# Kernel tuning notes

Hardware: AMD Instinct MI355X
Metric: run time of the kernel (lower is better)

## Reference

```python
import jax, jax.numpy as jnp
import numpy as np

HEADS = 16
DIM_HEAD = 64
SCALE = DIM_HEAD ** -0.5


def setup_inputs() -> dict:
    key = jax.random.key(0)
    ks = jax.random.split(key, 5)
    B, N, D = 2, 2048, 1024  # query_dim = inner_dim = 1024
    s = 0.02
    return {
        "x": jax.random.normal(ks[0], (B, N, D), dtype=jnp.float32),
        "Wq": jax.random.normal(ks[1], (D, D), dtype=jnp.float32) * s,
        "Wk": jax.random.normal(ks[2], (D, D), dtype=jnp.float32) * s,
        "Wv": jax.random.normal(ks[3], (D, D), dtype=jnp.float32) * s,
        "Wout": jax.random.normal(ks[4], (D, D), dtype=jnp.float32) * s,
        "bout": jnp.zeros((D,), dtype=jnp.float32),
    }


def reference(x, Wq, Wk, Wv, Wout, bout):
    B, N, D = x.shape
    h, dh = HEADS, DIM_HEAD
    # projections (torch Linear: y = x @ W.T); context = x (self-attention)
    q = (x @ Wq.T).reshape(B, N, h, dh).transpose(0, 2, 1, 3)  # b h n d
    k = (x @ Wk.T).reshape(B, N, h, dh).transpose(0, 2, 1, 3)
    v = (x @ Wv.T).reshape(B, N, h, dh).transpose(0, 2, 1, 3)
    # scaled dot-product attention; chunk loop in original is math-equivalent
    s = jnp.einsum('bhid,bhjd->bhij', q, k) * SCALE
    p = jax.nn.softmax(s, axis=-1)
    o = jnp.einsum('bhij,bhjd->bhid', p, v)  # b h n d
    o = o.transpose(0, 2, 1, 3).reshape(B, N, h * dh)
    return o @ Wout.T + bout
```

## Files before the change

kernel.cpp:

```cpp
#include <hip/hip_runtime.h>
#include <stdint.h>

using bf16x8 = __attribute__((ext_vector_type(8))) short;
using f32x4  = __attribute__((ext_vector_type(4))) float;
using s16x4  = __attribute__((ext_vector_type(4))) short;

__device__ __forceinline__ short f2bf(float f) {
    union { float f; uint32_t u; } v; v.f = f;
    uint32_t u = v.u;
    uint32_t r = (u + 0x7fffu + ((u >> 16) & 1u)) >> 16;
    return (short)r;
}

__device__ __forceinline__ uint32_t cvtpk_bf16(float a, float b) {
    uint32_t r;
    asm("v_cvt_pk_bf16_f32 %0, %1, %2" : "=v"(r) : "v"(a), "v"(b));
    return r;
}

__device__ __forceinline__ void gload_lds16(const void* g, void* l) {
    __builtin_amdgcn_global_load_lds(
        reinterpret_cast<const uint32_t __attribute__((address_space(1)))*>(
            reinterpret_cast<uintptr_t>(g)),
        reinterpret_cast<uint32_t __attribute__((address_space(3)))*>(
            reinterpret_cast<uintptr_t>(l)),
        16, 0, 0);
}

__global__ __launch_bounds__(256) void cvt_all(
    const float* __restrict__ x, const float* __restrict__ wq,
    const float* __restrict__ wk, const float* __restrict__ wv,
    const float* __restrict__ wo,
    short* __restrict__ xb, short* __restrict__ wqb, short* __restrict__ wkb,
    short* __restrict__ wvb, short* __restrict__ wob)
{
    int i = blockIdx.x * 256 + threadIdx.x;
    const float* src; short* dst; int off;
    if      (i < 1048576) { src = x;  dst = xb;  off = i; }
    else if (i < 1310720) { src = wq; dst = wqb; off = i - 1048576; }
    else if (i < 1572864) { src = wk; dst = wkb; off = i - 1310720; }
    else if (i < 1835008) { src = wv; dst = wvb; off = i - 1572864; }
    else                  { src = wo; dst = wob; off = i - 1835008; }
    float4 f = ((const float4*)src)[off];
    s16x4 r; r[0] = f2bf(f.x); r[1] = f2bf(f.y); r[2] = f2bf(f.z); r[3] = f2bf(f.w);
    ((s16x4*)dst)[off] = r;
}

template <bool IS_OUT>
__global__ __launch_bounds__(256) void gemm_bt(
    const short* __restrict__ A,
    const short* __restrict__ Bq, const short* __restrict__ Bk,
    const short* __restrict__ Bv,
    short* __restrict__ qb, short* __restrict__ kb, short* __restrict__ vtb,
    float* __restrict__ outp, const float* __restrict__ bias)
{
    constexpr int BN = IS_OUT ? 64 : 128;
    constexpr int BC = BN / 32;
    constexpr int NI = BN / 32;
    __shared__ short As[2][128 * 64];
    __shared__ short Bs[2][BN * 64];
    const int tid  = threadIdx.x;
    const int wave = tid >> 6, lane = tid & 63;
    const int lo = lane & 15, hi = lane >> 4;

    const int nwg = gridDim.x * gridDim.y * gridDim.z;
    int lin = blockIdx.x + blockIdx.y * gridDim.x +
              blockIdx.z * gridDim.x * gridDim.y;
    const int s = (lin & 7) * (nwg >> 3) + (lin >> 3);
    const int m_base = IS_OUT ? ((s >> 4) & 31) * 128 : ((s >> 3) & 31) * 128;
    const int n_base = IS_OUT ? (s & 15) * 64        : (s & 7) * 128;
    const int z = IS_OUT ? 0 : (s >> 8);

    const short* Bw = IS_OUT ? Bq : (z == 0 ? Bq : (z == 1 ? Bk : Bv));
    const int wr = wave >> 1, wc = wave & 1;

    f32x4 acc[4][NI];
#pragma unroll
    for (int i = 0; i < 4; ++i)
#pragma unroll
        for (int j = 0; j < NI; ++j) acc[i][j] = (f32x4){0.f, 0.f, 0.f, 0.f};

    const int se = (lane & 7) * 8;
    const short* Ag = A  + (size_t)(m_base + wave * 32 + (lane >> 3)) * 1024 + se;
    const short* Bg = Bw + (size_t)(n_base + wave * (BN / 4) + (lane >> 3)) * 1024 + se;

    auto GSTAGE = [&](int kt) {
        const int k0 = kt * 64, bf = kt & 1;
#pragma unroll
        for (int c = 0; c < 4; ++c)
            gload_lds16(Ag + (size_t)c * 8 * 1024 + k0, &As[bf][(wave * 32 + c * 8) * 64]);
#pragma unroll
        for (int c = 0; c < BC; ++c)
            gload_lds16(Bg + (size_t)c * 8 * 1024 + k0,
                        &Bs[bf][(wave * (BN / 4) + c * 8) * 64]);
    };

    GSTAGE(0);
    for (int kt = 0; kt < 16; ++kt) {
        if (kt < 15) {
            GSTAGE(kt + 1);
            if constexpr (IS_OUT)
                asm volatile("s_waitcnt vmcnt(6)" ::: "memory");
            else
                asm volatile("s_waitcnt vmcnt(8)" ::: "memory");
        } else {
            asm volatile("s_waitcnt vmcnt(0)" ::: "memory");
        }
        __builtin_amdgcn_s_barrier();
        const int bf = kt & 1;
#pragma unroll
        for (int ks = 0; ks < 2; ++ks) {
            bf16x8 av[4], bv[NI];
#pragma unroll
            for (int i = 0; i < 4; ++i)
                av[i] = *(const bf16x8*)&As[bf][(wr * 64 + i * 16 + lo) * 64 + ks * 32 + hi * 8];
#pragma unroll
            for (int i = 0; i < NI; ++i)
                bv[i] = *(const bf16x8*)&Bs[bf][(wc * (BN / 2) + i * 16 + lo) * 64 + ks * 32 + hi * 8];
#pragma unroll
            for (int mi = 0; mi < 4; ++mi)
#pragma unroll
                for (int ni = 0; ni < NI; ++ni)
                    acc[mi][ni] = __builtin_amdgcn_mfma_f32_16x16x32_bf16(
                        av[mi], bv[ni], acc[mi][ni], 0, 0, 0);
        }
        asm volatile("s_waitcnt lgkmcnt(0)" ::: "memory");
        __builtin_amdgcn_s_barrier();
    }

#pragma unroll
    for (int mi = 0; mi < 4; ++mi) {
#pragma unroll
        for (int ni = 0; ni < NI; ++ni) {
            const int n = n_base + wc * (BN / 2) + ni * 16 + lo;
            if (IS_OUT) {
                const float bsv = bias[n];
#pragma unroll
                for (int i = 0; i < 4; ++i) {
                    const int m = m_base + wr * 64 + mi * 16 + hi * 4 + i;
                    outp[(size_t)m * 1024 + n] = acc[mi][ni][i] + bsv;
                }
            } else {
                const int h = n >> 6, d = n & 63;
                if (z == 2) {
                    const int m0 = m_base + wr * 64 + mi * 16 + hi * 4;
                    const int b = m0 >> 11, ns = m0 & 2047;
                    const int k6 = ns & 63;
                    const int nsp = (ns & ~63) | (k6 & 0x20) |
                                    ((k6 & 0x10) >> 2) | ((k6 & 0x0C) << 1);
                    s16x4 pk;
#pragma unroll
                    for (int i = 0; i < 4; ++i) pk[i] = f2bf(acc[mi][ni][i]);
                    *(s16x4*)&vtb[(((size_t)b * 16 + h) * 64 + d) * 2048 + nsp] = pk;
                } else {
                    short* dstp = (z == 0) ? qb : kb;
                    const float scl = (z == 0) ? 0.18033688011112042f : 1.0f;
#pragma unroll
                    for (int i = 0; i < 4; ++i) {
                        const int m = m_base + wr * 64 + mi * 16 + hi * 4 + i;
                        const int b = m >> 11, ns = m & 2047;
                        dstp[(((size_t)b * 16 + h) * 2048 + ns) * 64 + d] =
                            f2bf(acc[mi][ni][i] * scl);
                    }
                }
            }
        }
    }
}


#define QKT16B_(BUFN, S) do {                                                  \
    const char* kb_ = (const char*)K_lds[BUFN];                                \
    bf16x8 kf_[4];                                                             \
    _Pragma("unroll")                                                          \
    for (int mi = 0; mi < 4; ++mi)                                             \
        kf_[mi] = *(const bf16x8*)(kb_ + koff0 + mi * 2048);                   \
    _Pragma("unroll")                                                          \
    for (int mi = 0; mi < 4; ++mi)                                             \
        _Pragma("unroll")                                                      \
        for (int nf = 0; nf < 2; ++nf)                                         \
            S[mi][nf] = __builtin_amdgcn_mfma_f32_16x16x32_bf16(               \
                kf_[mi], qf[nf][0], Z4, 0, 0, 0);                              \
    _Pragma("unroll")                                                          \
    for (int mi = 0; mi < 4; ++mi)                                             \
        kf_[mi] = *(const bf16x8*)(kb_ + koff1 + mi * 2048);                   \
    _Pragma("unroll")                                                          \
    for (int mi = 0; mi < 4; ++mi)                                             \
        _Pragma("unroll")                                                      \
        for (int nf = 0; nf < 2; ++nf)                                         \
            S[mi][nf] = __builtin_amdgcn_mfma_f32_16x16x32_bf16(               \
                kf_[mi], qf[nf][1], S[mi][nf], 0, 0, 0);                       \
    } while (0)

#define STAGE_(T_, BUF_) do {                                                  \
    const size_t go_ = (size_t)(T_) * gstep;                                   \
    _Pragma("unroll")                                                          \
    for (int c = 0; c < 4; ++c) {                                              \
        void* dst_ = (stV == 0) ? (void*)&K_lds[BUF_][(rbase + c * 8) * 64]    \
                                : (void*)&V_lds[BUF_][(rbase + c * 8) * 64];   \
        gload_lds16(gp[c] + go_, dst_);                                        \
    } } while (0)

#define HALF16_(T, SC, SN, DOQ, BUFC, BUFN, BUFS, DOS) do {                    \
    asm volatile("s_waitcnt vmcnt(0)" ::: "memory");                           \
    __builtin_amdgcn_s_barrier();                                              \
    if (DOQ) {                                                                 \
        __builtin_amdgcn_s_setprio(1);                                         \
        QKT16B_(BUFN, SN);                                                     \
        __builtin_amdgcn_s_setprio(0);                                         \
    }                                                                          \
    if (DOS) STAGE_((T) + 2, BUFS);            \
                          \
    float pm_[2];                                                              \
    _Pragma("unroll")                                                          \
    for (int nf = 0; nf < 2; ++nf) {                                           \
        float a0 = fmaxf(fmaxf(SC[0][nf][0], SC[0][nf][1]),                    \
                         fmaxf(SC[0][nf][2], SC[0][nf][3]));                   \
        float a1 = fmaxf(fmaxf(SC[1][nf][0], SC[1][nf][1]),                    \
                         fmaxf(SC[1][nf][2], SC[1][nf][3]));                   \
        float a2 = fmaxf(fmaxf(SC[2][nf][0], SC[2][nf][1]),                    \
                         fmaxf(SC[2][nf][2], SC[2][nf][3]));                   \
        float a3 = fmaxf(fmaxf(SC[3][nf][0], SC[3][nf][1]),                    \
                         fmaxf(SC[3][nf][2], SC[3][nf][3]));                   \
        pm_[nf] = fmaxf(fmaxf(a0, a1), fmaxf(a2, a3));                         \
    }                                                                          \
    const int keep_ = (pm_[0] <= mrow[0] + 8.f) && (pm_[1] <= mrow[1] + 8.f);  \
    if (!__all(keep_)) {                  \
        float alpha_[2];                                                       \
        _Pragma("unroll")                                                      \
        for (int nf = 0; nf < 2; ++nf) {                                       \
            float m4 = pm_[nf];                                                \
            m4 = fmaxf(m4, __shfl_xor(m4, 16));                                \
            m4 = fmaxf(m4, __shfl_xor(m4, 32));                                \
            const float mn = fmaxf(mrow[nf], m4);                              \
            alpha_[nf] = __builtin_amdgcn_exp2f(mrow[nf] - mn);                \
            mrow[nf]  = mn;                                                    \
            lrow[nf] *= alpha_[nf];                                            \
        }                                                                      \
        _Pragma("unroll")                                                      \
        for (int mi = 0; mi < 2; ++mi)                                         \
            _Pragma("unroll")                                                  \
            for (int i = 0; i < 4; ++i) {                                      \
                const float av = __shfl(alpha_[mi], hi * 4 + i);               \
                _Pragma("unroll")                                              \
                for (int nf = 0; nf < 4; ++nf) oacc[mi][nf][i] *= av;          \
            }                                                                  \
    }                                                                          \
    _Pragma("unroll")                                                          \
    for (int nf = 0; nf < 2; ++nf) {        \
        float s0 = 0.f, s1 = 0.f, s2 = 0.f, s3 = 0.f;                          \
        _Pragma("unroll")                                                      \
        for (int mi = 0; mi < 4; ++mi) {                                       \
            SC[mi][nf][0] = __builtin_amdgcn_exp2f(SC[mi][nf][0] - mrow[nf]);  \
            s0 += SC[mi][nf][0];                                               \
            SC[mi][nf][1] = __builtin_amdgcn_exp2f(SC[mi][nf][1] - mrow[nf]);  \
            s1 += SC[mi][nf][1];                                               \
            SC[mi][nf][2] = __builtin_amdgcn_exp2f(SC[mi][nf][2] - mrow[nf]);  \
            s2 += SC[mi][nf][2];                                               \
            SC[mi][nf][3] = __builtin_amdgcn_exp2f(SC[mi][nf][3] - mrow[nf]);  \
            s3 += SC[mi][nf][3];                                               \
        }                                                                      \
        lrow[nf] += (s0 + s1) + (s2 + s3);                                     \
    }                                                                          \
                 \
    uint32_t W2_[4][2][2];                                                     \
    _Pragma("unroll")                                                          \
    for (int mi = 0; mi < 4; ++mi)                                             \
        _Pragma("unroll")                                                      \
        for (int nf = 0; nf < 2; ++nf) {                                       \
            W2_[mi][nf][0] = cvtpk_bf16(SC[mi][nf][0], SC[mi][nf][1]);         \
            W2_[mi][nf][1] = cvtpk_bf16(SC[mi][nf][2], SC[mi][nf][3]);         \
        }                                                                      \
           \
    __builtin_amdgcn_s_setprio(1);                                             \
    _Pragma("unroll")                                                          \
    for (int ks = 0; ks < 2; ++ks) {                                           \
        const char* vb_ = (const char*)V_lds[BUFC];                            \
        bf16x8 vf_[4];                                                         \
        _Pragma("unroll")                                                      \
        for (int nf = 0; nf < 4; ++nf)                                         \
            vf_[nf] = *(const bf16x8*)(vb_ + (ks ? koff1 : koff0) + nf * 2048);\
        _Pragma("unroll")                                                      \
        for (int mo = 0; mo < 2; ++mo) {                                       \
            union { uint32_t u[4]; bf16x8 v; } pk_;                            \
            pk_.u[0] = W2_[ks * 2][mo][0];     pk_.u[1] = W2_[ks * 2][mo][1];  \
            pk_.u[2] = W2_[ks * 2 + 1][mo][0]; pk_.u[3] = W2_[ks * 2 + 1][mo][1]; \
            _Pragma("unroll")                                                  \
            for (int nf = 0; nf < 4; ++nf)                                     \
                oacc[mo][nf] = __builtin_amdgcn_mfma_f32_16x16x32_bf16(        \
                    pk_.v, vf_[nf], oacc[mo][nf], 0, 0, 0);                    \
        }                                                                      \
    }                                                                          \
    __builtin_amdgcn_s_setprio(0);                                             \
    } while (0)

__global__ __launch_bounds__(256) void attn(
    const short* __restrict__ qg, const short* __restrict__ kg,
    const short* __restrict__ vtg, short* __restrict__ ob)
{
    __shared__ short K_lds[3][64 * 64];
    __shared__ short V_lds[3][64 * 64];

    const int tid  = threadIdx.x;
    const int wave = tid >> 6, lane = tid & 63;
    const int lo = lane & 15, hi = lane >> 4;
    const int koff0 = lo * 128 + ((hi ^ (lo & 7)) << 4);
    const int koff1 = koff0 ^ 64;

    int bid = blockIdx.y * 16 + blockIdx.x;
    bid = (bid & 7) * 64 + (bid >> 3);
    const int bh = bid >> 4;
    const int qw = (bid & 15) * 128 + wave * 32;

    bf16x8 qf[2][2];
#pragma unroll
    for (int nf = 0; nf < 2; ++nf)
#pragma unroll
        for (int ks = 0; ks < 2; ++ks)
            qf[nf][ks] = *(const bf16x8*)&qg[((size_t)bh * 2048 + qw + nf * 16 + lo) * 64 +
                                             ks * 32 + hi * 8];
    asm volatile("s_waitcnt vmcnt(0)" ::: "memory");

    f32x4 oacc[2][4];
#pragma unroll
    for (int mi = 0; mi < 2; ++mi)
#pragma unroll
        for (int nf = 0; nf < 4; ++nf) oacc[mi][nf] = (f32x4){0.f, 0.f, 0.f, 0.f};
    float mrow[2] = {-1e30f, -1e30f};
    float lrow[2] = {0.f, 0.f};
    const f32x4 Z4 = (f32x4){0.f, 0.f, 0.f, 0.f};

    const short* kgb = kg  + (size_t)bh * 2048 * 64;
    const short* vgb = vtg + (size_t)bh * 64 * 2048;

    const int stV = wave >> 1, rbase = (wave & 1) * 32;
    const short* gp[4];
#pragma unroll
    for (int c = 0; c < 4; ++c) {
        const int r  = rbase + c * 8 + (lane >> 3);
        const int sg = (lane & 7) ^ (r & 7);
        gp[c] = (stV == 0) ? (kgb + (size_t)r * 64 + sg * 8)
                           : (vgb + (size_t)r * 2048 + sg * 8);
    }
    const int gstep = (stV == 0) ? 4096 : 64;

    STAGE_(0, 0); STAGE_(1, 1);

    f32x4 sA[4][2], sB[4][2];

    asm volatile("s_waitcnt vmcnt(4)" ::: "memory");
    __builtin_amdgcn_s_barrier();
    QKT16B_(0, sA);

    for (int tb = 0; tb < 30; tb += 6) {
        HALF16_(tb + 0, sA, sB, 1, 0, 1, 2, 1);
        HALF16_(tb + 1, sB, sA, 1, 1, 2, 0, 1);
        HALF16_(tb + 2, sA, sB, 1, 2, 0, 1, 1);
        HALF16_(tb + 3, sB, sA, 1, 0, 1, 2, 1);
        HALF16_(tb + 4, sA, sB, 1, 1, 2, 0, 1);
        HALF16_(tb + 5, sB, sA, 1, 2, 0, 1, 1);
    }
    HALF16_(30, sA, sB, 1, 0, 1, 2, 0);
    HALF16_(31, sB, sA, 0, 1, 2, 0, 0);

    float lfull[2];
#pragma unroll
    for (int nf = 0; nf < 2; ++nf) {
        float ts = lrow[nf];
        ts += __shfl_xor(ts, 16);
        ts += __shfl_xor(ts, 32);
        lfull[nf] = ts;
    }
    const int b = bh >> 4, h = bh & 15;
#pragma unroll
    for (int mi = 0; mi < 2; ++mi)
#pragma unroll
        for (int i = 0; i < 4; ++i) {
            const float lv = __shfl(lfull[mi], hi * 4 + i);
            const float r  = 1.0f / lv;
            const int qrow = qw + mi * 16 + hi * 4 + i;
#pragma unroll
            for (int nf = 0; nf < 4; ++nf)
                ob[((size_t)b * 2048 + qrow) * 1024 + h * 64 + nf * 16 + lo] =
                    f2bf(oacc[mi][nf][i] * r);
        }
}

extern "C" void kernel_launch(void* const* d_in, const int* in_sizes, int n_in,
                              void* d_out, int out_size, void* d_ws, size_t ws_size,
                              hipStream_t stream) {
    const float* x   = (const float*)d_in[0];
    const float* Wq  = (const float*)d_in[1];
    const float* Wk  = (const float*)d_in[2];
    const float* Wv  = (const float*)d_in[3];
    const float* Wo  = (const float*)d_in[4];
    const float* bo  = (const float*)d_in[5];
    float* outp = (float*)d_out;

    char* ws = (char*)d_ws;
    short* xb  = (short*)(ws);
    short* qb  = (short*)(ws + (8u  << 20));
    short* kb  = (short*)(ws + (16u << 20));
    short* vtb = (short*)(ws + (24u << 20));
    short* ob  = (short*)(ws + (32u << 20));
    short* wqb = (short*)(ws + (40u << 20));
    short* wkb = (short*)(ws + (42u << 20));
    short* wvb = (short*)(ws + (44u << 20));
    short* wob = (short*)(ws + (46u << 20));

    cvt_all<<<8192, 256, 0, stream>>>(x, Wq, Wk, Wv, Wo, xb, wqb, wkb, wvb, wob);
    gemm_bt<false><<<dim3(8, 32, 3), 256, 0, stream>>>(
        xb, wqb, wkb, wvb, qb, kb, vtb, nullptr, nullptr);
    attn<<<dim3(16, 32), 256, 0, stream>>>(qb, kb, vtb, ob);
    gemm_bt<true><<<dim3(16, 32, 1), 256, 0, stream>>>(
        ob, wob, nullptr, nullptr, nullptr, nullptr, nullptr, outp, bo);
}
```

Measured before the change: 123.6 us.

## Decouple K and V staging with a shorter V prefetch distance

K and V tiles now load through separate staging macros. K keeps a triple buffer prefetched two iterations ahead, while V uses a double buffer prefetched one iteration ahead. This cuts LDS use (one fewer V buffer) and may allow higher occupancy, but V loads have less time to land before they are consumed. The buffer index schedule in the unrolled loop is rewritten to match.

```diff
diff --git a/kernel.cpp b/kernel.cpp
--- a/kernel.cpp
+++ b/kernel.cpp
@@ -192,24 +192,32 @@
                 kf_[mi], qf[nf][1], S[mi][nf], 0, 0, 0);                       \
     } while (0)
 
-#define STAGE_(T_, BUF_) do {                                                  \
-    const size_t go_ = (size_t)(T_) * gstep;                                   \
-    _Pragma("unroll")                                                          \
-    for (int c = 0; c < 4; ++c) {                                              \
-        void* dst_ = (stV == 0) ? (void*)&K_lds[BUF_][(rbase + c * 8) * 64]    \
-                                : (void*)&V_lds[BUF_][(rbase + c * 8) * 64];   \
-        gload_lds16(gp[c] + go_, dst_);                                        \
+#define STAGEK_(T_, BUF_) do {                                                 \
+    if (stV == 0) {                                                            \
+        const size_t go_ = (size_t)(T_) * 4096;                                \
+        _Pragma("unroll")                                                      \
+        for (int c = 0; c < 4; ++c)                                            \
+            gload_lds16(gp[c] + go_, &K_lds[BUF_][(rbase + c * 8) * 64]);      \
     } } while (0)
 
-#define HALF16_(T, SC, SN, DOQ, BUFC, BUFN, BUFS, DOS) do {                    \
+#define STAGEV_(T_, BUF_) do {                                                 \
+    if (stV == 1) {                                                            \
+        const size_t go_ = (size_t)(T_) * 64;                                  \
+        _Pragma("unroll")                                                      \
+        for (int c = 0; c < 4; ++c)                                            \
+            gload_lds16(gp[c] + go_, &V_lds[BUF_][(rbase + c * 8) * 64]);      \
+    } } while (0)
+
+#define HALF16_(T, SC, SN, DOQ, BUFCV, BUFNK, BUFSK, BUFSV, DOSK, DOSV) do {   \
     asm volatile("s_waitcnt vmcnt(0)" ::: "memory");                           \
     __builtin_amdgcn_s_barrier();                                              \
     if (DOQ) {                                                                 \
         __builtin_amdgcn_s_setprio(1);                                         \
-        QKT16B_(BUFN, SN);                                                     \
+        QKT16B_(BUFNK, SN);                                                    \
         __builtin_amdgcn_s_setprio(0);                                         \
     }                                                                          \
-    if (DOS) STAGE_((T) + 2, BUFS);            \
+    if (DOSK) STAGEK_((T) + 2, BUFSK);         \
+    if (DOSV) STAGEV_((T) + 1, BUFSV);                                         \
                           \
     float pm_[2];                                                              \
     _Pragma("unroll")                                                          \
@@ -275,7 +283,7 @@
     __builtin_amdgcn_s_setprio(1);                                             \
     _Pragma("unroll")                                                          \
     for (int ks = 0; ks < 2; ++ks) {                                           \
-        const char* vb_ = (const char*)V_lds[BUFC];                            \
+        const char* vb_ = (const char*)V_lds[BUFCV];                           \
         bf16x8 vf_[4];                                                         \
         _Pragma("unroll")                                                      \
         for (int nf = 0; nf < 4; ++nf)                                         \
@@ -299,7 +307,7 @@
     const short* __restrict__ vtg, short* __restrict__ ob)
 {
     __shared__ short K_lds[3][64 * 64];
-    __shared__ short V_lds[3][64 * 64];
+    __shared__ short V_lds[2][64 * 64];
 
     const int tid  = threadIdx.x;
     const int wave = tid >> 6, lane = tid & 63;
@@ -342,9 +350,8 @@
         gp[c] = (stV == 0) ? (kgb + (size_t)r * 64 + sg * 8)
                            : (vgb + (size_t)r * 2048 + sg * 8);
     }
-    const int gstep = (stV == 0) ? 4096 : 64;
-
-    STAGE_(0, 0); STAGE_(1, 1);
+
+    STAGEK_(0, 0); STAGEV_(0, 0); STAGEK_(1, 1);
 
     f32x4 sA[4][2], sB[4][2];
 
@@ -353,15 +360,15 @@
     QKT16B_(0, sA);
 
     for (int tb = 0; tb < 30; tb += 6) {
-        HALF16_(tb + 0, sA, sB, 1, 0, 1, 2, 1);
-        HALF16_(tb + 1, sB, sA, 1, 1, 2, 0, 1);
-        HALF16_(tb + 2, sA, sB, 1, 2, 0, 1, 1);
-        HALF16_(tb + 3, sB, sA, 1, 0, 1, 2, 1);
-        HALF16_(tb + 4, sA, sB, 1, 1, 2, 0, 1);
-        HALF16_(tb + 5, sB, sA, 1, 2, 0, 1, 1);
+        HALF16_(tb + 0, sA, sB, 1, 0, 1, 2, 1, 1, 1);
+        HALF16_(tb + 1, sB, sA, 1, 1, 2, 0, 0, 1, 1);
+        HALF16_(tb + 2, sA, sB, 1, 0, 0, 1, 1, 1, 1);
+        HALF16_(tb + 3, sB, sA, 1, 1, 1, 2, 0, 1, 1);
+        HALF16_(tb + 4, sA, sB, 1, 0, 2, 0, 1, 1, 1);
+        HALF16_(tb + 5, sB, sA, 1, 1, 0, 1, 0, 1, 1);
     }
-    HALF16_(30, sA, sB, 1, 0, 1, 2, 0);
-    HALF16_(31, sB, sA, 0, 1, 2, 0, 0);
+    HALF16_(30, sA, sB, 1, 0, 1, 0, 1, 0, 1);
+    HALF16_(31, sB, sA, 0, 1, 0, 0, 0, 0, 0);
 
     float lfull[2];
 #pragma unroll
```

Measured after the change: 141.1 us. 1.14x slower.
